# Performance work log

Measured on AMD Instinct MI355X. Metric: run time of the kernel, lower is better.

Reference implementation:

```python
import jax, jax.numpy as jnp
import numpy as np

D = 256; NH = 8; NLEV = 4; NPTS = 4; DH = D // NH
DFFN = 1024; B = 8; LQ = 900
SHAPES = np.array([[100, 100], [50, 50], [25, 25], [13, 13]], dtype=np.int64)
STARTS = np.concatenate([[0], np.cumsum(SHAPES[:, 0] * SHAPES[:, 1])[:-1]]).astype(np.int64)
LEN = int((SHAPES[:, 0] * SHAPES[:, 1]).sum())


def _ln(x, w, b, eps=1e-5):
    m = x.mean(-1, keepdims=True)
    v = ((x - m) ** 2).mean(-1, keepdims=True)
    return (x - m) / jnp.sqrt(v + eps) * w + b


def _msdeform(q, ref, src, val_w, val_b, off_w, off_b, aw_w, aw_b, op_w, op_b):
    # Multi-scale deformable attention (Deformable DETR core), grid_sample
    # bilinear / zeros padding / align_corners=False semantics.
    Bq, Lq = q.shape[0], q.shape[1]
    value = (src @ val_w + val_b).reshape(Bq, -1, NH, DH)
    off = (q @ off_w + off_b).reshape(Bq, Lq, NH, NLEV, NPTS, 2)
    aw = jax.nn.softmax((q @ aw_w + aw_b).reshape(Bq, Lq, NH, NLEV * NPTS), -1)
    aw = aw.reshape(Bq, Lq, NH, NLEV, NPTS)
    norm = jnp.asarray(SHAPES[:, ::-1].copy(), dtype=q.dtype)  # (W_l, H_l)
    loc = ref[:, :, None, :, None, :] + off / norm[None, None, None, :, None, :]
    out = jnp.zeros((Bq, Lq, NH, DH), q.dtype)
    for l in range(NLEV):
        Hl, Wl = int(SHAPES[l, 0]), int(SHAPES[l, 1]); s = int(STARTS[l])
        v = value[:, s:s + Hl * Wl]                  # [B, Hl*Wl, NH, DH]
        lx = loc[:, :, :, l, :, 0] * Wl - 0.5        # align_corners=False pixel coords
        ly = loc[:, :, :, l, :, 1] * Hl - 0.5        # [B, Lq, NH, NPTS]
        x0 = jnp.floor(lx); y0 = jnp.floor(ly)
        fx = lx - x0; fy = ly - y0
        x0 = x0.astype(jnp.int32); y0 = y0.astype(jnp.int32)
        samp = jnp.zeros((Bq, Lq, NH, NPTS, DH), q.dtype)
        for dx, dy in ((0, 0), (1, 0), (0, 1), (1, 1)):
            xi = x0 + dx; yi = y0 + dy
            w = (fx if dx else 1.0 - fx) * (fy if dy else 1.0 - fy)
            valid = (xi >= 0) & (xi < Wl) & (yi >= 0) & (yi < Hl)
            idx = jnp.clip(yi, 0, Hl - 1) * Wl + jnp.clip(xi, 0, Wl - 1)
            idx_f = idx.transpose(0, 1, 3, 2).reshape(Bq, Lq * NPTS, NH)
            g = jnp.take_along_axis(v, idx_f[..., None], axis=1)
            g = g.reshape(Bq, Lq, NPTS, NH, DH).transpose(0, 1, 3, 2, 4)
            samp = samp + jnp.where(valid, w, 0.0)[..., None] * g
        out = out + jnp.sum(samp * aw[:, :, :, l, :, None], axis=3)
    return out.reshape(Bq, Lq, D) @ op_w + op_b


def _forward(tgt, query_pos, reference_points, src, qkv_w, qkv_b, out_w, out_b,
             ln2_w, ln2_b, val_w, val_b, off_w, off_b, aw_w, aw_b, op_w, op_b,
             ln1_w, ln1_b, w1, b1, w2, b2, ln3_w, ln3_b):
    Bq, Lq, _ = tgt.shape
    # --- self attention: q=k=tgt+pos, value=tgt (eval mode, no dropout) ---
    q = tgt + query_pos
    wq, wk, wv = qkv_w[:, :D], qkv_w[:, D:2 * D], qkv_w[:, 2 * D:]
    bq, bk, bv = qkv_b[:D], qkv_b[D:2 * D], qkv_b[2 * D:]
    qh = (q @ wq + bq).reshape(Bq, Lq, NH, DH)
    kh = (q @ wk + bk).reshape(Bq, Lq, NH, DH)
    vh = (tgt @ wv + bv).reshape(Bq, Lq, NH, DH)
    scores = jnp.einsum('bqhd,bkhd->bhqk', qh, kh) / jnp.sqrt(jnp.asarray(DH, tgt.dtype))
    attn = jax.nn.softmax(scores, -1)
    sa = jnp.einsum('bhqk,bkhd->bqhd', attn, vh).reshape(Bq, Lq, D) @ out_w + out_b
    tgt = _ln(tgt + sa, ln2_w, ln2_b)
    # --- multi-scale deformable cross attention ---
    ca = _msdeform(tgt + query_pos, reference_points, src,
                   val_w, val_b, off_w, off_b, aw_w, aw_b, op_w, op_b)
    tgt = _ln(tgt + ca, ln1_w, ln1_b)
    # --- FFN ---
    ff = jax.nn.relu(tgt @ w1 + b1) @ w2 + b2
    return _ln(tgt + ff, ln3_w, ln3_b)


def setup_inputs():
    key = jax.random.key(0)
    ks = jax.random.split(key, 16)
    s = 0.02
    return {
        'tgt': jax.random.normal(ks[0], (B, LQ, D), jnp.float32),
        'query_pos': jax.random.normal(ks[1], (B, LQ, D), jnp.float32),
        'reference_points': jax.random.uniform(ks[2], (B, LQ, NLEV, 2), jnp.float32),
        'src': jax.random.normal(ks[3], (B, LEN, D), jnp.float32),
        'spatial_shapes': jnp.asarray(SHAPES),
        'level_start_index': jnp.asarray(STARTS),
        'qkv_w': jax.random.normal(ks[4], (D, 3 * D), jnp.float32) * s,
        'qkv_b': jnp.zeros((3 * D,), jnp.float32),
        'out_w': jax.random.normal(ks[5], (D, D), jnp.float32) * s,
        'out_b': jnp.zeros((D,), jnp.float32),
        'ln2_w': jnp.ones((D,), jnp.float32), 'ln2_b': jnp.zeros((D,), jnp.float32),
        'val_w': jax.random.normal(ks[6], (D, D), jnp.float32) * s,
        'val_b': jnp.zeros((D,), jnp.float32),
        'off_w': jax.random.normal(ks[7], (D, NH * NLEV * NPTS * 2), jnp.float32) * s,
        'off_b': jax.random.normal(ks[8], (NH * NLEV * NPTS * 2,), jnp.float32) * 0.5,
        'aw_w': jax.random.normal(ks[9], (D, NH * NLEV * NPTS), jnp.float32) * s,
        'aw_b': jnp.zeros((NH * NLEV * NPTS,), jnp.float32),
        'op_w': jax.random.normal(ks[10], (D, D), jnp.float32) * s,
        'op_b': jnp.zeros((D,), jnp.float32),
        'ln1_w': jnp.ones((D,), jnp.float32), 'ln1_b': jnp.zeros((D,), jnp.float32),
        'w1': jax.random.normal(ks[11], (D, DFFN), jnp.float32) * s,
        'b1': jnp.zeros((DFFN,), jnp.float32),
        'w2': jax.random.normal(ks[12], (DFFN, D), jnp.float32) * s,
        'b2': jnp.zeros((D,), jnp.float32),
        'ln3_w': jnp.ones((D,), jnp.float32), 'ln3_b': jnp.zeros((D,), jnp.float32),
    }


def reference(tgt, query_pos, reference_points, src, spatial_shapes, level_start_index,
              qkv_w, qkv_b, out_w, out_b, ln2_w, ln2_b, val_w, val_b, off_w, off_b,
              aw_w, aw_b, op_w, op_b, ln1_w, ln1_b, w1, b1, w2, b2, ln3_w, ln3_b):
    return _forward(tgt, query_pos, reference_points, src, qkv_w, qkv_b, out_w, out_b,
                    ln2_w, ln2_b, val_w, val_b, off_w, off_b, aw_w, aw_b, op_w, op_b,
                    ln1_w, ln1_b, w1, b1, w2, b2, ln3_w, ln3_b)
```

## Files before the change

kernel.cpp:

```cpp
#include <hip/hip_runtime.h>
#include <math.h>

#define Dm    256
#define NHm   8
#define DHm   32
#define NLEVm 4
#define NPTSm 4
#define DFFNm 1024
#define Bm    8
#define LQm   900
#define LENm  13294
#define MQ    (Bm * LQm)
#define MV    (Bm * LENm)
#define MQP   7296
#define MVP   106368
#define LQP   960

typedef __attribute__((ext_vector_type(8))) short short8;
typedef __attribute__((ext_vector_type(4))) float f32x4;

__device__ __forceinline__ unsigned short f2bf(float f) {
    unsigned int b = __float_as_uint(f);
    unsigned int r = (b + 0x7FFFu + ((b >> 16) & 1u)) >> 16;
    return (unsigned short)r;
}
__device__ __forceinline__ float bf2f(unsigned short u) {
    return __uint_as_float(((unsigned int)u) << 16);
}

__global__ __launch_bounds__(256) void prep0(const float* __restrict__ tgt,
                                             const float* __restrict__ qpos,
                                             unsigned short* __restrict__ tgtb,
                                             unsigned short* __restrict__ qb,
                                             int n4, int n4pad) {
    int i = blockIdx.x * blockDim.x + threadIdx.x;
    int stride = gridDim.x * blockDim.x;
    for (; i < n4pad; i += stride) {
        ushort4 ut, uq;
        if (i < n4) {
            float4 x = reinterpret_cast<const float4*>(tgt)[i];
            float4 y = reinterpret_cast<const float4*>(qpos)[i];
            ut.x = f2bf(x.x); ut.y = f2bf(x.y); ut.z = f2bf(x.z); ut.w = f2bf(x.w);
            uq.x = f2bf(x.x + y.x); uq.y = f2bf(x.y + y.y);
            uq.z = f2bf(x.z + y.z); uq.w = f2bf(x.w + y.w);
        } else {
            ut.x = ut.y = ut.z = ut.w = 0;
            uq.x = uq.y = uq.z = uq.w = 0;
        }
        reinterpret_cast<ushort4*>(tgtb)[i] = ut;
        reinterpret_cast<ushort4*>(qb)[i] = uq;
    }
}

__global__ __launch_bounds__(256) void vtpad_kernel(unsigned short* __restrict__ vt) {
    int i = blockIdx.x * 256 + threadIdx.x;
    int row = i / 60, c = 900 + (i % 60);
    vt[(size_t)row * LQP + c] = 0;
}

__device__ __forceinline__ void wt_tile(const float* __restrict__ W,
                                        unsigned short* __restrict__ BT,
                                        int N, int K, int n0, int k0, int t,
                                        float (*tile)[65]) {
    #pragma unroll
    for (int r0 = 0; r0 < 64; r0 += 16) {
        int r = r0 + (t >> 4);
        int c = (t & 15) * 4;
        float4 v = *reinterpret_cast<const float4*>(W + (size_t)(k0 + r) * N + n0 + c);
        tile[r][c + 0] = v.x; tile[r][c + 1] = v.y; tile[r][c + 2] = v.z; tile[r][c + 3] = v.w;
    }
    __syncthreads();
    #pragma unroll
    for (int s = t; s < 512; s += 256) {
        int r = s >> 3, c8 = (s & 7) * 8;
        short8 u;
        #pragma unroll
        for (int j = 0; j < 8; ++j) u[j] = (short)f2bf(tile[c8 + j][r]);
        *reinterpret_cast<short8*>(BT + (size_t)(n0 + r) * K + k0 + c8) = u;
    }
}

__global__ __launch_bounds__(256) void wt_all(
        const float* __restrict__ qkv_w, const float* __restrict__ out_w,
        const float* __restrict__ val_w, const float* __restrict__ off_w,
        const float* __restrict__ aw_w,  const float* __restrict__ op_w,
        const float* __restrict__ w1,    const float* __restrict__ w2,
        unsigned short* __restrict__ BT_qkv, unsigned short* __restrict__ BT_out,
        unsigned short* __restrict__ BT_val, unsigned short* __restrict__ BT_off,
        unsigned short* __restrict__ BT_aw,  unsigned short* __restrict__ BT_op,
        unsigned short* __restrict__ BT_w1,  unsigned short* __restrict__ BT_w2) {
    __shared__ float tile[64][65];
    int bid = blockIdx.x;
    int t = threadIdx.x;
    const float* W; unsigned short* BT; int N, K, idx;
    if      (bid < 48)  { W = qkv_w; BT = BT_qkv; N = 768;  K = 256;  idx = bid; }
    else if (bid < 64)  { W = out_w; BT = BT_out; N = 256;  K = 256;  idx = bid - 48; }
    else if (bid < 80)  { W = val_w; BT = BT_val; N = 256;  K = 256;  idx = bid - 64; }
    else if (bid < 96)  { W = off_w; BT = BT_off; N = 256;  K = 256;  idx = bid - 80; }
    else if (bid < 104) { W = aw_w;  BT = BT_aw;  N = 128;  K = 256;  idx = bid - 96; }
    else if (bid < 120) { W = op_w;  BT = BT_op;  N = 256;  K = 256;  idx = bid - 104; }
    else if (bid < 184) { W = w1;    BT = BT_w1;  N = 1024; K = 256;  idx = bid - 120; }
    else                { W = w2;    BT = BT_w2;  N = 256;  K = 1024; idx = bid - 184; }
    int nt = N / 64;
    int n0 = (idx % nt) * 64, k0 = (idx / nt) * 64;
    wt_tile(W, BT, N, K, n0, k0, t, tile);
}

template <int RELU, int OBF>
__global__ __launch_bounds__(256) void bgemm(int M, int N, int K,
        const unsigned short* __restrict__ A,
        const unsigned short* __restrict__ BT,
        const float* __restrict__ bias, const float* __restrict__ bias2,
        float* __restrict__ Cf, float* __restrict__ Cf2,
        unsigned short* __restrict__ Cb, int ldc) {
    __shared__ __align__(16) unsigned short As[2][128 * 32];
    __shared__ __align__(16) unsigned short Bs[2][128 * 32];
    int t = threadIdx.x;
    int l = t & 63;
    int w = t >> 6;
    int row0 = blockIdx.x * 128, col0 = blockIdx.y * 128;
    int wr = (w >> 1) * 64, wc = (w & 1) * 64;
    f32x4 acc[4][4];
    #pragma unroll
    for (int m = 0; m < 4; ++m)
        #pragma unroll
        for (int n = 0; n < 4; ++n) acc[m][n] = (f32x4){0.f, 0.f, 0.f, 0.f};

    int s0 = t, s1 = t + 256;
    const unsigned short* Ag = A + (size_t)row0 * K;
    const unsigned short* Bg = BT + (size_t)col0 * K;
    const unsigned short* a0p = Ag + (size_t)(s0 >> 2) * K + (s0 & 3) * 8;
    const unsigned short* a1p = Ag + (size_t)(s1 >> 2) * K + (s1 & 3) * 8;
    const unsigned short* b0p = Bg + (size_t)(s0 >> 2) * K + (s0 & 3) * 8;
    const unsigned short* b1p = Bg + (size_t)(s1 >> 2) * K + (s1 & 3) * 8;

    short8 ra0 = *(const short8*)(a0p);
    short8 ra1 = *(const short8*)(a1p);
    short8 rb0 = *(const short8*)(b0p);
    short8 rb1 = *(const short8*)(b1p);

    int cur = 0;
    for (int k0 = 0; k0 < K; k0 += 32) {
        unsigned short* Ac = As[cur];
        unsigned short* Bc = Bs[cur];
        *(short8*)(Ac + s0 * 8) = ra0;
        *(short8*)(Ac + s1 * 8) = ra1;
        *(short8*)(Bc + s0 * 8) = rb0;
        *(short8*)(Bc + s1 * 8) = rb1;
        if (k0 + 32 < K) {
            ra0 = *(const short8*)(a0p + k0 + 32);
            ra1 = *(const short8*)(a1p + k0 + 32);
            rb0 = *(const short8*)(b0p + k0 + 32);
            rb1 = *(const short8*)(b1p + k0 + 32);
        }
        __syncthreads();
        short8 af[4], bfr[4];
        #pragma unroll
        for (int m = 0; m < 4; ++m)
            af[m] = *(const short8*)(Ac + (wr + m * 16 + (l & 15)) * 32 + (l >> 4) * 8);
        #pragma unroll
        for (int n = 0; n < 4; ++n)
            bfr[n] = *(const short8*)(Bc + (wc + n * 16 + (l & 15)) * 32 + (l >> 4) * 8);
        #pragma unroll
        for (int m = 0; m < 4; ++m)
            #pragma unroll
            for (int n = 0; n < 4; ++n)
                acc[m][n] = __builtin_amdgcn_mfma_f32_16x16x32_bf16(af[m], bfr[n], acc[m][n], 0, 0, 0);
        cur ^= 1;
    }

    int cr = (l >> 4) * 4;
    int cc = l & 15;
    #pragma unroll
    for (int m = 0; m < 4; ++m) {
        #pragma unroll
        for (int n = 0; n < 4; ++n) {
            int col = col0 + wc + n * 16 + cc;
            if (OBF == 2) {
                float bv = bias[col];
                int r0 = row0 + wr + m * 16 + cr;
                if (r0 < M) {
                    int bb = r0 / 900;
                    int q = r0 - bb * 900;
                    ushort4 u;
                    u.x = f2bf(acc[m][n][0] + bv);
                    u.y = f2bf(acc[m][n][1] + bv);
                    u.z = f2bf(acc[m][n][2] + bv);
                    u.w = f2bf(acc[m][n][3] + bv);
                    *reinterpret_cast<ushort4*>(Cb + ((size_t)(bb * 256 + col)) * LQP + q) = u;
                }
            } else if (OBF == 3) {
                float bv = (col < 256) ? bias[col] : bias2[col - 256];
                #pragma unroll
                for (int j = 0; j < 4; ++j) {
                    int r = row0 + wr + m * 16 + cr + j;
                    if (r < M) {
                        float v = acc[m][n][j] + bv;
                        if (col < 256) Cf[(size_t)r * 256 + col] = v;
                        else           Cf2[(size_t)r * 128 + (col - 256)] = v;
                    }
                }
            } else {
                float bv = bias[col];
                #pragma unroll
                for (int j = 0; j < 4; ++j) {
                    int r = row0 + wr + m * 16 + cr + j;
                    if (r < M) {
                        float v = acc[m][n][j] + bv;
                        if (RELU) v = fmaxf(v, 0.f);
                        if (OBF) Cb[(size_t)r * ldc + col] = f2bf(v);
                        else     Cf[(size_t)r * ldc + col] = v;
                    }
                }
            }
        }
    }
}

__global__ __launch_bounds__(256) void bgemm_vf(int M, int N, int K,
        const float* __restrict__ A,
        const unsigned short* __restrict__ BT,
        const float* __restrict__ bias,
        unsigned short* __restrict__ Cb, int ldc) {
    __shared__ __align__(16) unsigned short As[2][128 * 32];
    __shared__ __align__(16) unsigned short Bs[2][128 * 32];
    int t = threadIdx.x;
    int l = t & 63;
    int w = t >> 6;
    int row0 = blockIdx.x * 128, col0 = blockIdx.y * 128;
    int wr = (w >> 1) * 64, wc = (w & 1) * 64;
    f32x4 acc[4][4];
    #pragma unroll
    for (int m = 0; m < 4; ++m)
        #pragma unroll
        for (int n = 0; n < 4; ++n) acc[m][n] = (f32x4){0.f, 0.f, 0.f, 0.f};

    int s0 = t, s1 = t + 256;
    int r0c = min(row0 + (s0 >> 2), M - 1);
    int r1c = min(row0 + (s1 >> 2), M - 1);
    const float* a0p = A + (size_t)r0c * K + (s0 & 3) * 8;
    const float* a1p = A + (size_t)r1c * K + (s1 & 3) * 8;
    const unsigned short* Bg = BT + (size_t)col0 * K;
    const unsigned short* b0p = Bg + (size_t)(s0 >> 2) * K + (s0 & 3) * 8;
    const unsigned short* b1p = Bg + (size_t)(s1 >> 2) * K + (s1 & 3) * 8;

    float4 fa0 = *(const float4*)(a0p);
    float4 fa1 = *(const float4*)(a0p + 4);
    float4 fb0 = *(const float4*)(a1p);
    float4 fb1 = *(const float4*)(a1p + 4);
    short8 rb0 = *(const short8*)(b0p);
    short8 rb1 = *(const short8*)(b1p);

    int cur = 0;
    for (int k0 = 0; k0 < K; k0 += 32) {
        unsigned short* Ac = As[cur];
        unsigned short* Bc = Bs[cur];
        short8 ra0, ra1;
        ra0[0] = (short)f2bf(fa0.x); ra0[1] = (short)f2bf(fa0.y);
        ra0[2] = (short)f2bf(fa0.z); ra0[3] = (short)f2bf(fa0.w);
        ra0[4] = (short)f2bf(fa1.x); ra0[5] = (short)f2bf(fa1.y);
        ra0[6] = (short)f2bf(fa1.z); ra0[7] = (short)f2bf(fa1.w);
        ra1[0] = (short)f2bf(fb0.x); ra1[1] = (short)f2bf(fb0.y);
        ra1[2] = (short)f2bf(fb0.z); ra1[3] = (short)f2bf(fb0.w);
        ra1[4] = (short)f2bf(fb1.x); ra1[5] = (short)f2bf(fb1.y);
        ra1[6] = (short)f2bf(fb1.z); ra1[7] = (short)f2bf(fb1.w);
        *(short8*)(Ac + s0 * 8) = ra0;
        *(short8*)(Ac + s1 * 8) = ra1;
        *(short8*)(Bc + s0 * 8) = rb0;
        *(short8*)(Bc + s1 * 8) = rb1;
        if (k0 + 32 < K) {
            fa0 = *(const float4*)(a0p + k0 + 32);
            fa1 = *(const float4*)(a0p + k0 + 36);
            fb0 = *(const float4*)(a1p + k0 + 32);
            fb1 = *(const float4*)(a1p + k0 + 36);
            rb0 = *(const short8*)(b0p + k0 + 32);
            rb1 = *(const short8*)(b1p + k0 + 32);
        }
        __syncthreads();
        short8 af[4], bfr[4];
        #pragma unroll
        for (int m = 0; m < 4; ++m)
            af[m] = *(const short8*)(Ac + (wr + m * 16 + (l & 15)) * 32 + (l >> 4) * 8);
        #pragma unroll
        for (int n = 0; n < 4; ++n)
            bfr[n] = *(const short8*)(Bc + (wc + n * 16 + (l & 15)) * 32 + (l >> 4) * 8);
        #pragma unroll
        for (int m = 0; m < 4; ++m)
            #pragma unroll
            for (int n = 0; n < 4; ++n)
                acc[m][n] = __builtin_amdgcn_mfma_f32_16x16x32_bf16(af[m], bfr[n], acc[m][n], 0, 0, 0);
        cur ^= 1;
    }

    int cr = (l >> 4) * 4;
    int cc = l & 15;
    #pragma unroll
    for (int m = 0; m < 4; ++m) {
        #pragma unroll
        for (int n = 0; n < 4; ++n) {
            int col = col0 + wc + n * 16 + cc;
            float bv = bias[col];
            #pragma unroll
            for (int j = 0; j < 4; ++j) {
                int r = row0 + wr + m * 16 + cr + j;
                if (r < M)
                    Cb[(size_t)r * ldc + col] = f2bf(acc[m][n][j] + bv);
            }
        }
    }
}

__global__ __launch_bounds__(256) void flash_mfma(const unsigned short* __restrict__ qk,
                                                  const unsigned short* __restrict__ vt,
                                                  unsigned short* __restrict__ out) {
    __shared__ unsigned short P_lds[4][16][72];
    int t = threadIdx.x;
    int l = t & 63, w = t >> 6;
    int lr = l & 15, lg = l >> 4;
    int qt = blockIdx.x, h = blockIdx.y, b = blockIdx.z;
    const float scale = 0.17677669529663687f;

    short8 qf = *(const short8*)(qk + (size_t)(b * LQm + qt * 64 + w * 16 + lr) * 512 + h * 32 + lg * 8);

    f32x4 accO[2];
    accO[0] = (f32x4){0.f, 0.f, 0.f, 0.f};
    accO[1] = (f32x4){0.f, 0.f, 0.f, 0.f};
    float mrow[4] = {-1e30f, -1e30f, -1e30f, -1e30f};
    float lrow[4] = {0.f, 0.f, 0.f, 0.f};
    const f32x4 zero = (f32x4){0.f, 0.f, 0.f, 0.f};
    const unsigned short* vtb = vt + ((size_t)(b * 256 + h * 32)) * LQP;

    for (int kt = 0; kt < 15; ++kt) {
        int k0 = kt * 64;
        f32x4 sfr[4];
        #pragma unroll
        for (int ks = 0; ks < 4; ++ks) {
            short8 kf = *(const short8*)(qk + (size_t)(b * LQm + k0 + ks * 16 + lr) * 512 + 256 + h * 32 + lg * 8);
            sfr[ks] = __builtin_amdgcn_mfma_f32_16x16x32_bf16(qf, kf, zero, 0, 0, 0);
        }
        float sv[4][4];
        #pragma unroll
        for (int ks = 0; ks < 4; ++ks) {
            bool valid = (k0 + ks * 16 + lr) < LQm;
            #pragma unroll
            for (int j = 0; j < 4; ++j)
                sv[ks][j] = valid ? sfr[ks][j] * scale : -1e30f;
        }
        float tm[4], newm[4], rr[4], ps[4];
        #pragma unroll
        for (int j = 0; j < 4; ++j)
            tm[j] = fmaxf(fmaxf(sv[0][j], sv[1][j]), fmaxf(sv[2][j], sv[3][j]));
        #pragma unroll
        for (int msk = 1; msk <= 8; msk <<= 1) {
            #pragma unroll
            for (int j = 0; j < 4; ++j) tm[j] = fmaxf(tm[j], __shfl_xor(tm[j], msk));
        }
        #pragma unroll
        for (int j = 0; j < 4; ++j) {
            newm[j] = fmaxf(mrow[j], tm[j]);
            rr[j] = __expf(mrow[j] - newm[j]);
            mrow[j] = newm[j];
            ps[j] = 0.f;
        }
        float pv[4][4];
        #pragma unroll
        for (int ks = 0; ks < 4; ++ks)
            #pragma unroll
            for (int j = 0; j < 4; ++j) {
                pv[ks][j] = __expf(sv[ks][j] - newm[j]);
                ps[j] += pv[ks][j];
            }
        #pragma unroll
        for (int msk = 1; msk <= 8; msk <<= 1) {
            #pragma unroll
            for (int j = 0; j < 4; ++j) ps[j] += __shfl_xor(ps[j], msk);
        }
        #pragma unroll
        for (int j = 0; j < 4; ++j) lrow[j] = lrow[j] * rr[j] + ps[j];
        #pragma unroll
        for (int n = 0; n < 2; ++n)
            #pragma unroll
            for (int j = 0; j < 4; ++j) accO[n][j] *= rr[j];
        #pragma unroll
        for (int ks = 0; ks < 4; ++ks)
            #pragma unroll
            for (int j = 0; j < 4; ++j)
                P_lds[w][lg * 4 + j][ks * 16 + lr] = f2bf(pv[ks][j]);
        #pragma unroll
        for (int kh2 = 0; kh2 < 2; ++kh2) {
            short8 pf = *(const short8*)(&P_lds[w][lr][kh2 * 32 + lg * 8]);
            #pragma unroll
            for (int n = 0; n < 2; ++n) {
                short8 vf = *(const short8*)(vtb + (size_t)(n * 16 + lr) * LQP + k0 + kh2 * 32 + lg * 8);
                accO[n] = __builtin_amdgcn_mfma_f32_16x16x32_bf16(pf, vf, accO[n], 0, 0, 0);
            }
        }
    }
    float inv[4];
    #pragma unroll
    for (int j = 0; j < 4; ++j) inv[j] = 1.0f / lrow[j];
    #pragma unroll
    for (int n = 0; n < 2; ++n)
        #pragma unroll
        for (int j = 0; j < 4; ++j) {
            int q = qt * 64 + w * 16 + lg * 4 + j;
            if (q < LQm)
                out[(size_t)(b * LQm + q) * 256 + h * 32 + n * 16 + lr] = f2bf(accO[n][j] * inv[j]);
        }
}

template <int DUAL, int QP>
__global__ __launch_bounds__(256) void add_ln_kernel(const float* __restrict__ x,
                                                     const float* __restrict__ r,
                                                     const float* __restrict__ w,
                                                     const float* __restrict__ b,
                                                     const float* __restrict__ qpos,
                                                     float* __restrict__ out,
                                                     unsigned short* __restrict__ outb,
                                                     unsigned short* __restrict__ outq) {
    int row = blockIdx.x * 4 + (threadIdx.x >> 6);
    int lane = threadIdx.x & 63;
    size_t i4 = (size_t)row * 64 + lane;
    float4 xv = reinterpret_cast<const float4*>(x)[i4];
    float4 rv = reinterpret_cast<const float4*>(r)[i4];
    float4 v = make_float4(xv.x + rv.x, xv.y + rv.y, xv.z + rv.z, xv.w + rv.w);
    float s = v.x + v.y + v.z + v.w;
    #pragma unroll
    for (int msk = 1; msk <= 32; msk <<= 1) s += __shfl_xor(s, msk);
    float mean = s * (1.0f / Dm);
    float4 dv = make_float4(v.x - mean, v.y - mean, v.z - mean, v.w - mean);
    float sq = dv.x * dv.x + dv.y * dv.y + dv.z * dv.z + dv.w * dv.w;
    #pragma unroll
    for (int msk = 1; msk <= 32; msk <<= 1) sq += __shfl_xor(sq, msk);
    float is = rsqrtf(sq * (1.0f / Dm) + 1e-5f);
    float4 wv = reinterpret_cast<const float4*>(w)[lane];
    float4 bv = reinterpret_cast<const float4*>(b)[lane];
    float4 res = make_float4(dv.x * is * wv.x + bv.x, dv.y * is * wv.y + bv.y,
                             dv.z * is * wv.z + bv.z, dv.w * is * wv.w + bv.w);
    reinterpret_cast<float4*>(out)[i4] = res;
    if (DUAL) {
        ushort4 u;
        u.x = f2bf(res.x); u.y = f2bf(res.y); u.z = f2bf(res.z); u.w = f2bf(res.w);
        reinterpret_cast<ushort4*>(outb)[i4] = u;
    }
    if (QP) {
        float4 qv = reinterpret_cast<const float4*>(qpos)[i4];
        ushort4 u;
        u.x = f2bf(res.x + qv.x); u.y = f2bf(res.y + qv.y);
        u.z = f2bf(res.z + qv.z); u.w = f2bf(res.w + qv.w);
        reinterpret_cast<ushort4*>(outq)[i4] = u;
    }
}

__global__ __launch_bounds__(256) void msdeform_kernel(const unsigned short* __restrict__ value,
                                                       const float* __restrict__ ref,
                                                       const float* __restrict__ off,
                                                       const float* __restrict__ awl,
                                                       unsigned short* __restrict__ out) {
    const int HL[4] = {100, 50, 25, 13};
    const int ST[4] = {0, 10000, 12500, 13125};
    __shared__ float lsx[4][128], lsy[4][128], wtab[4][128];
    __shared__ float2 ctab[4][512];
    int wv = threadIdx.x >> 6, lane = threadIdx.x & 63;
    int m = blockIdx.x * 4 + wv;
    int b = m / LQm;

    #pragma unroll
    for (int e = lane; e < 128; e += 64) {
        int lev = (e >> 2) & 3;
        float rx = ref[((size_t)m * NLEVm + lev) * 2 + 0];
        float ry = ref[((size_t)m * NLEVm + lev) * 2 + 1];
        float ox = off[(size_t)m * 256 + e * 2 + 0];
        float oy = off[(size_t)m * 256 + e * 2 + 1];
        float Wf = (float)HL[lev];
        lsx[wv][e] = (rx + ox / Wf) * Wf - 0.5f;
        lsy[wv][e] = (ry + oy / Wf) * Wf - 0.5f;
        wtab[wv][e] = awl[(size_t)m * 128 + e];
    }
    __syncthreads();
    if (lane < NHm) {
        int h = lane;
        float mx = -1e30f;
        #pragma unroll
        for (int i = 0; i < 16; i++) mx = fmaxf(mx, wtab[wv][h * 16 + i]);
        float s = 0.f;
        #pragma unroll
        for (int i = 0; i < 16; i++) {
            float e = __expf(wtab[wv][h * 16 + i] - mx);
            wtab[wv][h * 16 + i] = e; s += e;
        }
        float inv = 1.0f / s;
        #pragma unroll
        for (int i = 0; i < 16; i++) wtab[wv][h * 16 + i] *= inv;
    }
    __syncthreads();
    #pragma unroll
    for (int j = 0; j < 8; ++j) {
        int e2 = lane * 8 + j;
        int c = e2 & 3, e = e2 >> 2;
        int lev = (e >> 2) & 3;
        int Wl = HL[lev];
        float lx = lsx[wv][e], ly = lsy[wv][e];
        float x0f = floorf(lx), y0f = floorf(ly);
        float fx = lx - x0f, fy = ly - y0f;
        int dx = c & 1, dy = c >> 1;
        int xi = (int)x0f + dx, yi = (int)y0f + dy;
        bool valid = (xi >= 0) && (xi < Wl) && (yi >= 0) && (yi < Wl);
        float wc = valid ? ((dx ? fx : 1.0f - fx) * (dy ? fy : 1.0f - fy)) * wtab[wv][e] : 0.f;
        int xc = min(max(xi, 0), Wl - 1), yc = min(max(yi, 0), Wl - 1);
        int row = b * LENm + ST[lev] + yc * Wl + xc;
        ctab[wv][e2] = make_float2(__int_as_float(row), wc);
    }
    __syncthreads();
    int h = lane >> 3, dg = lane & 7;
    const unsigned short* basep = value + h * 32 + dg * 4;
    float a0 = 0.f, a1 = 0.f, a2 = 0.f, a3 = 0.f;
    #pragma unroll
    for (int i = 0; i < 16; ++i) {
        #pragma unroll
        for (int c = 0; c < 4; ++c) {
            float2 cc = ctab[wv][(h * 16 + i) * 4 + c];
            int row = __float_as_int(cc.x);
            float wc = cc.y;
            ushort4 v = *reinterpret_cast<const ushort4*>(basep + (size_t)row * 256);
            a0 += wc * bf2f(v.x); a1 += wc * bf2f(v.y);
            a2 += wc * bf2f(v.z); a3 += wc * bf2f(v.w);
        }
    }
    ushort4 o;
    o.x = f2bf(a0); o.y = f2bf(a1); o.z = f2bf(a2); o.w = f2bf(a3);
    *reinterpret_cast<ushort4*>(out + (size_t)m * 256 + h * 32 + dg * 4) = o;
}

extern "C" void kernel_launch(void* const* d_in, const int* in_sizes, int n_in,
                              void* d_out, int out_size, void* d_ws, size_t ws_size,
                              hipStream_t stream) {
    const float* tgt   = (const float*)d_in[0];
    const float* qpos  = (const float*)d_in[1];
    const float* refp  = (const float*)d_in[2];
    const float* src   = (const float*)d_in[3];
    const float* qkv_w = (const float*)d_in[6];
    const float* qkv_b = (const float*)d_in[7];
    const float* out_w = (const float*)d_in[8];
    const float* out_b = (const float*)d_in[9];
    const float* ln2_w = (const float*)d_in[10];
    const float* ln2_b = (const float*)d_in[11];
    const float* val_w = (const float*)d_in[12];
    const float* val_b = (const float*)d_in[13];
    const float* off_w = (const float*)d_in[14];
    const float* off_b = (const float*)d_in[15];
    const float* aw_w  = (const float*)d_in[16];
    const float* aw_b  = (const float*)d_in[17];
    const float* op_w  = (const float*)d_in[18];
    const float* op_b  = (const float*)d_in[19];
    const float* ln1_w = (const float*)d_in[20];
    const float* ln1_b = (const float*)d_in[21];
    const float* w1    = (const float*)d_in[22];
    const float* b1    = (const float*)d_in[23];
    const float* w2    = (const float*)d_in[24];
    const float* b2    = (const float*)d_in[25];
    const float* ln3_w = (const float*)d_in[26];
    const float* ln3_b = (const float*)d_in[27];

    char* base = (char*)d_ws;
    unsigned short* value_bf  = (unsigned short*)(base);
    unsigned short* hidden_bf = (unsigned short*)(base + 54460416);
    unsigned short* t2_bf     = (unsigned short*)(base + 54460416 + 14942208);
    unsigned short* qk_bf = (unsigned short*)(base + 108920832);
    float* offb = (float*)(base + 108920832);
    float* awb  = (float*)(base + 108920832 + 7372800);
    unsigned short* Vt = (unsigned short*)(base + 123666432);
    float* S1   = (float*)(base + 123666432);
    float* t1   = (float*)(base + 131039232);
    float* t2   = (float*)(base + 138412032);
    unsigned short* Qbf     = (unsigned short*)(base + 145784832);
    unsigned short* tgt_bf  = (unsigned short*)(base + 149520384);
    unsigned short* attn_bf = (unsigned short*)(base + 153255936);
    unsigned short* ca_bf   = (unsigned short*)(base + 156991488);
    unsigned short* BT_qkv  = (unsigned short*)(base + 160727040);
    unsigned short* BT_out  = BT_qkv + 768 * 256;
    unsigned short* BT_val  = BT_out + 256 * 256;
    unsigned short* BT_off  = BT_val + 256 * 256;
    unsigned short* BT_aw   = BT_off + 256 * 256;
    unsigned short* BT_op   = BT_aw + 128 * 256;
    unsigned short* BT_w1   = BT_op + 256 * 256;
    unsigned short* BT_w2   = BT_w1 + 1024 * 256;
    float* outp = (float*)d_out;

    dim3 blk(256);
    wt_all<<<dim3(248), blk, 0, stream>>>(qkv_w, out_w, val_w, off_w, aw_w, op_w, w1, w2,
                                          BT_qkv, BT_out, BT_val, BT_off, BT_aw, BT_op, BT_w1, BT_w2);

    prep0<<<dim3(1824), blk, 0, stream>>>(tgt, qpos, tgt_bf, Qbf, MQ * Dm / 4, MQP * Dm / 4);

    bgemm<0, 1><<<dim3(57, 4), blk, 0, stream>>>(MQ, 512, 256, Qbf, BT_qkv, qkv_b, nullptr, nullptr, nullptr, qk_bf, 512);
    bgemm<0, 2><<<dim3(57, 2), blk, 0, stream>>>(MQ, 256, 256, tgt_bf, BT_qkv + 512 * 256, qkv_b + 512, nullptr, nullptr, nullptr, Vt, 256);
    vtpad_kernel<<<dim3(480), blk, 0, stream>>>(Vt);
    flash_mfma<<<dim3(15, NHm, Bm), blk, 0, stream>>>(qk_bf, Vt, attn_bf);
    bgemm<0, 0><<<dim3(57, 2), blk, 0, stream>>>(MQ, 256, 256, attn_bf, BT_out, out_b, nullptr, S1, nullptr, nullptr, 256);
    add_ln_kernel<0, 1><<<dim3(1800), blk, 0, stream>>>(tgt, S1, ln2_w, ln2_b, qpos, t1, nullptr, Qbf);
    bgemm_vf<<<dim3(831, 2), blk, 0, stream>>>(MV, 256, 256, src, BT_val, val_b, value_bf, 256);
    bgemm<0, 3><<<dim3(57, 3), blk, 0, stream>>>(MQ, 384, 256, Qbf, BT_off, off_b, aw_b, offb, awb, nullptr, 0);
    msdeform_kernel<<<dim3(1800), blk, 0, stream>>>(value_bf, refp, offb, awb, ca_bf);
    bgemm<0, 0><<<dim3(57, 2), blk, 0, stream>>>(MQ, 256, 256, ca_bf, BT_op, op_b, nullptr, S1, nullptr, nullptr, 256);
    add_ln_kernel<1, 0><<<dim3(1800), blk, 0, stream>>>(t1, S1, ln1_w, ln1_b, nullptr, t2, t2_bf, nullptr);
    bgemm<1, 1><<<dim3(57, 8), blk, 0, stream>>>(MQ, DFFNm, 256, t2_bf, BT_w1, b1, nullptr, nullptr, nullptr, hidden_bf, DFFNm);
    bgemm<0, 0><<<dim3(57, 2), blk, 0, stream>>>(MQ, 256, 1024, hidden_bf, BT_w2, b2, nullptr, S1, nullptr, nullptr, 256);
    add_ln_kernel<0, 0><<<dim3(1800), blk, 0, stream>>>(t2, S1, ln3_w, ln3_b, nullptr, outp, nullptr, nullptr);
}
```

Before: 265.9 us.

## Merge value, QK, V-transpose GEMMs and Vt padding into one launch

Combines the large value projection GEMM, the Q/K projection GEMM, the transposed V projection GEMM, and the Vt padding zeroing into a single kernel that dispatches on block index. This removes three kernel launches and lets the small QK/V GEMMs share the GPU with the big value GEMM, filling otherwise underutilised CUs. The value GEMM is moved earlier in the schedule, since it does not depend on the self-attention branch. The cost is a larger, more register-heavy kernel with divergent roles per block.

```diff
diff --git a/kernel.cpp b/kernel.cpp
--- a/kernel.cpp
+++ b/kernel.cpp
@@ -50,12 +50,6 @@
         reinterpret_cast<ushort4*>(tgtb)[i] = ut;
         reinterpret_cast<ushort4*>(qb)[i] = uq;
     }
-}
-
-__global__ __launch_bounds__(256) void vtpad_kernel(unsigned short* __restrict__ vt) {
-    int i = blockIdx.x * 256 + threadIdx.x;
-    int row = i / 60, c = 900 + (i % 60);
-    vt[(size_t)row * LQP + c] = 0;
 }
 
 __device__ __forceinline__ void wt_tile(const float* __restrict__ W,
@@ -106,6 +100,22 @@
     wt_tile(W, BT, N, K, n0, k0, t, tile);
 }
 
+__device__ __forceinline__ void mfma_step(const unsigned short* Ac, const unsigned short* Bc,
+                                          int wr, int wc, int l, f32x4 acc[4][4]) {
+    short8 af[4], bfr[4];
+    #pragma unroll
+    for (int m = 0; m < 4; ++m)
+        af[m] = *(const short8*)(Ac + (wr + m * 16 + (l & 15)) * 32 + (l >> 4) * 8);
+    #pragma unroll
+    for (int n = 0; n < 4; ++n)
+        bfr[n] = *(const short8*)(Bc + (wc + n * 16 + (l & 15)) * 32 + (l >> 4) * 8);
+    #pragma unroll
+    for (int m = 0; m < 4; ++m)
+        #pragma unroll
+        for (int n = 0; n < 4; ++n)
+            acc[m][n] = __builtin_amdgcn_mfma_f32_16x16x32_bf16(af[m], bfr[n], acc[m][n], 0, 0, 0);
+}
+
 template <int RELU, int OBF>
 __global__ __launch_bounds__(256) void bgemm(int M, int N, int K,
         const unsigned short* __restrict__ A,
@@ -154,18 +164,7 @@
             rb1 = *(const short8*)(b1p + k0 + 32);
         }
         __syncthreads();
-        short8 af[4], bfr[4];
-        #pragma unroll
-        for (int m = 0; m < 4; ++m)
-            af[m] = *(const short8*)(Ac + (wr + m * 16 + (l & 15)) * 32 + (l >> 4) * 8);
-        #pragma unroll
-        for (int n = 0; n < 4; ++n)
-            bfr[n] = *(const short8*)(Bc + (wc + n * 16 + (l & 15)) * 32 + (l >> 4) * 8);
-        #pragma unroll
-        for (int m = 0; m < 4; ++m)
-            #pragma unroll
-            for (int n = 0; n < 4; ++n)
-                acc[m][n] = __builtin_amdgcn_mfma_f32_16x16x32_bf16(af[m], bfr[n], acc[m][n], 0, 0, 0);
+        mfma_step(Ac, Bc, wr, wc, l, acc);
         cur ^= 1;
     }
 
@@ -176,20 +175,7 @@
         #pragma unroll
         for (int n = 0; n < 4; ++n) {
             int col = col0 + wc + n * 16 + cc;
-            if (OBF == 2) {
-                float bv = bias[col];
-                int r0 = row0 + wr + m * 16 + cr;
-                if (r0 < M) {
-                    int bb = r0 / 900;
-                    int q = r0 - bb * 900;
-                    ushort4 u;
-                    u.x = f2bf(acc[m][n][0] + bv);
-                    u.y = f2bf(acc[m][n][1] + bv);
-                    u.z = f2bf(acc[m][n][2] + bv);
-                    u.w = f2bf(acc[m][n][3] + bv);
-                    *reinterpret_cast<ushort4*>(Cb + ((size_t)(bb * 256 + col)) * LQP + q) = u;
-                }
-            } else if (OBF == 3) {
+            if (OBF == 3) {
                 float bv = (col < 256) ? bias[col] : bias2[col - 256];
                 #pragma unroll
                 for (int j = 0; j < 4; ++j) {
@@ -217,94 +203,169 @@
     }
 }
 
-__global__ __launch_bounds__(256) void bgemm_vf(int M, int N, int K,
-        const float* __restrict__ A,
-        const unsigned short* __restrict__ BT,
-        const float* __restrict__ bias,
-        unsigned short* __restrict__ Cb, int ldc) {
+__global__ __launch_bounds__(256) void fused_gemms(
+        const float* __restrict__ src, const unsigned short* __restrict__ BT_val,
+        const float* __restrict__ val_b, unsigned short* __restrict__ value_bf,
+        const unsigned short* __restrict__ Qbf, const unsigned short* __restrict__ BT_qkv,
+        const float* __restrict__ qkv_b, unsigned short* __restrict__ qk_bf,
+        const unsigned short* __restrict__ tgt_bf, unsigned short* __restrict__ Vt) {
     __shared__ __align__(16) unsigned short As[2][128 * 32];
     __shared__ __align__(16) unsigned short Bs[2][128 * 32];
+    int bid = blockIdx.x;
     int t = threadIdx.x;
-    int l = t & 63;
-    int w = t >> 6;
-    int row0 = blockIdx.x * 128, col0 = blockIdx.y * 128;
+
+    if (bid >= 2004) {
+        int i = (bid - 2004) * 256 + t;
+        int row = i / 60, c = 900 + (i % 60);
+        Vt[(size_t)row * LQP + c] = 0;
+        return;
+    }
+
+    int l = t & 63, w = t >> 6;
     int wr = (w >> 1) * 64, wc = (w & 1) * 64;
+    int s0 = t, s1 = t + 256;
     f32x4 acc[4][4];
     #pragma unroll
     for (int m = 0; m < 4; ++m)
         #pragma unroll
         for (int n = 0; n < 4; ++n) acc[m][n] = (f32x4){0.f, 0.f, 0.f, 0.f};
-
-    int s0 = t, s1 = t + 256;
-    int r0c = min(row0 + (s0 >> 2), M - 1);
-    int r1c = min(row0 + (s1 >> 2), M - 1);
-    const float* a0p = A + (size_t)r0c * K + (s0 & 3) * 8;
-    const float* a1p = A + (size_t)r1c * K + (s1 & 3) * 8;
-    const unsigned short* Bg = BT + (size_t)col0 * K;
-    const unsigned short* b0p = Bg + (size_t)(s0 >> 2) * K + (s0 & 3) * 8;
-    const unsigned short* b1p = Bg + (size_t)(s1 >> 2) * K + (s1 & 3) * 8;
-
-    float4 fa0 = *(const float4*)(a0p);
-    float4 fa1 = *(const float4*)(a0p + 4);
-    float4 fb0 = *(const float4*)(a1p);
-    float4 fb1 = *(const float4*)(a1p + 4);
-    short8 rb0 = *(const short8*)(b0p);
-    short8 rb1 = *(const short8*)(b1p);
-
-    int cur = 0;
-    for (int k0 = 0; k0 < K; k0 += 32) {
-        unsigned short* Ac = As[cur];
-        unsigned short* Bc = Bs[cur];
-        short8 ra0, ra1;
-        ra0[0] = (short)f2bf(fa0.x); ra0[1] = (short)f2bf(fa0.y);
-        ra0[2] = (short)f2bf(fa0.z); ra0[3] = (short)f2bf(fa0.w);
-        ra0[4] = (short)f2bf(fa1.x); ra0[5] = (short)f2bf(fa1.y);
-        ra0[6] = (short)f2bf(fa1.z); ra0[7] = (short)f2bf(fa1.w);
-        ra1[0] = (short)f2bf(fb0.x); ra1[1] = (short)f2bf(fb0.y);
-        ra1[2] = (short)f2bf(fb0.z); ra1[3] = (short)f2bf(fb0.w);
-        ra1[4] = (short)f2bf(fb1.x); ra1[5] = (short)f2bf(fb1.y);
-        ra1[6] = (short)f2bf(fb1.z); ra1[7] = (short)f2bf(fb1.w);
-        *(short8*)(Ac + s0 * 8) = ra0;
-        *(short8*)(Ac + s1 * 8) = ra1;
-        *(short8*)(Bc + s0 * 8) = rb0;
-        *(short8*)(Bc + s1 * 8) = rb1;
-        if (k0 + 32 < K) {
-            fa0 = *(const float4*)(a0p + k0 + 32);
-            fa1 = *(const float4*)(a0p + k0 + 36);
-            fb0 = *(const float4*)(a1p + k0 + 32);
-            fb1 = *(const float4*)(a1p + k0 + 36);
-            rb0 = *(const short8*)(b0p + k0 + 32);
-            rb1 = *(const short8*)(b1p + k0 + 32);
-        }
-        __syncthreads();
-        short8 af[4], bfr[4];
-        #pragma unroll
-        for (int m = 0; m < 4; ++m)
-            af[m] = *(const short8*)(Ac + (wr + m * 16 + (l & 15)) * 32 + (l >> 4) * 8);
-        #pragma unroll
-        for (int n = 0; n < 4; ++n)
-            bfr[n] = *(const short8*)(Bc + (wc + n * 16 + (l & 15)) * 32 + (l >> 4) * 8);
-        #pragma unroll
-        for (int m = 0; m < 4; ++m)
-            #pragma unroll
-            for (int n = 0; n < 4; ++n)
-                acc[m][n] = __builtin_amdgcn_mfma_f32_16x16x32_bf16(af[m], bfr[n], acc[m][n], 0, 0, 0);
-        cur ^= 1;
-    }
-
     int cr = (l >> 4) * 4;
     int cc = l & 15;
-    #pragma unroll
-    for (int m = 0; m < 4; ++m) {
-        #pragma unroll
-        for (int n = 0; n < 4; ++n) {
-            int col = col0 + wc + n * 16 + cc;
-            float bv = bias[col];
-            #pragma unroll
-            for (int j = 0; j < 4; ++j) {
-                int r = row0 + wr + m * 16 + cr + j;
-                if (r < M)
-                    Cb[(size_t)r * ldc + col] = f2bf(acc[m][n][j] + bv);
+
+    if (bid < 1662) {
+        int row0 = (bid % 831) * 128, col0 = (bid / 831) * 128;
+        int r0c = min(row0 + (s0 >> 2), MV - 1);
+        int r1c = min(row0 + (s1 >> 2), MV - 1);
+        const float* a0p = src + (size_t)r0c * 256 + (s0 & 3) * 8;
+        const float* a1p = src + (size_t)r1c * 256 + (s1 & 3) * 8;
+        const unsigned short* Bg = BT_val + (size_t)col0 * 256;
+        const unsigned short* b0p = Bg + (size_t)(s0 >> 2) * 256 + (s0 & 3) * 8;
+        const unsigned short* b1p = Bg + (size_t)(s1 >> 2) * 256 + (s1 & 3) * 8;
+
+        float4 fa0 = *(const float4*)(a0p);
+        float4 fa1 = *(const float4*)(a0p + 4);
+        float4 fb0 = *(const float4*)(a1p);
+        float4 fb1 = *(const float4*)(a1p + 4);
+        short8 rb0 = *(const short8*)(b0p);
+        short8 rb1 = *(const short8*)(b1p);
+
+        int cur = 0;
+        for (int k0 = 0; k0 < 256; k0 += 32) {
+            unsigned short* Ac = As[cur];
+            unsigned short* Bc = Bs[cur];
+            short8 ra0, ra1;
+            ra0[0] = (short)f2bf(fa0.x); ra0[1] = (short)f2bf(fa0.y);
+            ra0[2] = (short)f2bf(fa0.z); ra0[3] = (short)f2bf(fa0.w);
+            ra0[4] = (short)f2bf(fa1.x); ra0[5] = (short)f2bf(fa1.y);
+            ra0[6] = (short)f2bf(fa1.z); ra0[7] = (short)f2bf(fa1.w);
+            ra1[0] = (short)f2bf(fb0.x); ra1[1] = (short)f2bf(fb0.y);
+            ra1[2] = (short)f2bf(fb0.z); ra1[3] = (short)f2bf(fb0.w);
+            ra1[4] = (short)f2bf(fb1.x); ra1[5] = (short)f2bf(fb1.y);
+            ra1[6] = (short)f2bf(fb1.z); ra1[7] = (short)f2bf(fb1.w);
+            *(short8*)(Ac + s0 * 8) = ra0;
+            *(short8*)(Ac + s1 * 8) = ra1;
+            *(short8*)(Bc + s0 * 8) = rb0;
+            *(short8*)(Bc + s1 * 8) = rb1;
+            if (k0 + 32 < 256) {
+                fa0 = *(const float4*)(a0p + k0 + 32);
+                fa1 = *(const float4*)(a0p + k0 + 36);
+                fb0 = *(const float4*)(a1p + k0 + 32);
+                fb1 = *(const float4*)(a1p + k0 + 36);
+                rb0 = *(const short8*)(b0p + k0 + 32);
+                rb1 = *(const short8*)(b1p + k0 + 32);
+            }
+            __syncthreads();
+            mfma_step(Ac, Bc, wr, wc, l, acc);
+            cur ^= 1;
+        }
+        #pragma unroll
+        for (int m = 0; m < 4; ++m) {
+            #pragma unroll
+            for (int n = 0; n < 4; ++n) {
+                int col = col0 + wc + n * 16 + cc;
+                float bv = val_b[col];
+                #pragma unroll
+                for (int j = 0; j < 4; ++j) {
+                    int r = row0 + wr + m * 16 + cr + j;
+                    if (r < MV)
+                        value_bf[(size_t)r * 256 + col] = f2bf(acc[m][n][j] + bv);
+                }
+            }
+        }
+    } else {
+        bool is_qk = (bid < 1890);
+        int idx = is_qk ? (bid - 1662) : (bid - 1890);
+        int row0 = (idx % 57) * 128;
+        int col0 = (idx / 57) * 128;
+        const unsigned short* A  = is_qk ? Qbf : tgt_bf;
+        const unsigned short* BT = is_qk ? BT_qkv : (BT_qkv + 512 * 256);
+        const float* bias        = is_qk ? qkv_b : (qkv_b + 512);
+
+        const unsigned short* Ag = A + (size_t)row0 * 256;
+        const unsigned short* Bg = BT + (size_t)col0 * 256;
+        const unsigned short* a0p = Ag + (size_t)(s0 >> 2) * 256 + (s0 & 3) * 8;
+        const unsigned short* a1p = Ag + (size_t)(s1 >> 2) * 256 + (s1 & 3) * 8;
+        const unsigned short* b0p = Bg + (size_t)(s0 >> 2) * 256 + (s0 & 3) * 8;
+        const unsigned short* b1p = Bg + (size_t)(s1 >> 2) * 256 + (s1 & 3) * 8;
+
+        short8 ra0 = *(const short8*)(a0p);
+        short8 ra1 = *(const short8*)(a1p);
+        short8 rb0 = *(const short8*)(b0p);
+        short8 rb1 = *(const short8*)(b1p);
+
+        int cur = 0;
+        for (int k0 = 0; k0 < 256; k0 += 32) {
+            unsigned short* Ac = As[cur];
+            unsigned short* Bc = Bs[cur];
+            *(short8*)(Ac + s0 * 8) = ra0;
+            *(short8*)(Ac + s1 * 8) = ra1;
+            *(short8*)(Bc + s0 * 8) = rb0;
+            *(short8*)(Bc + s1 * 8) = rb1;
+            if (k0 + 32 < 256) {
+                ra0 = *(const short8*)(a0p + k0 + 32);
+                ra1 = *(const short8*)(a1p + k0 + 32);
+                rb0 = *(const short8*)(b0p + k0 + 32);
+                rb1 = *(const short8*)(b1p + k0 + 32);
+            }
+            __syncthreads();
+            mfma_step(Ac, Bc, wr, wc, l, acc);
+            cur ^= 1;
+        }
+
+        if (is_qk) {
+            #pragma unroll
+            for (int m = 0; m < 4; ++m) {
+                #pragma unroll
+                for (int n = 0; n < 4; ++n) {
+                    int col = col0 + wc + n * 16 + cc;
+                    float bv = bias[col];
+                    #pragma unroll
+                    for (int j = 0; j < 4; ++j) {
+                        int r = row0 + wr + m * 16 + cr + j;
+                        if (r < MQ)
+                            qk_bf[(size_t)r * 512 + col] = f2bf(acc[m][n][j] + bv);
+                    }
+                }
+            }
+        } else {
+            #pragma unroll
+            for (int m = 0; m < 4; ++m) {
+                #pragma unroll
+                for (int n = 0; n < 4; ++n) {
+                    int col = col0 + wc + n * 16 + cc;
+                    float bv = bias[col];
+                    int r0 = row0 + wr + m * 16 + cr;
+                    if (r0 < MQ) {
+                        int bb = r0 / 900;
+                        int q = r0 - bb * 900;
+                        ushort4 u;
+                        u.x = f2bf(acc[m][n][0] + bv);
+                        u.y = f2bf(acc[m][n][1] + bv);
+                        u.z = f2bf(acc[m][n][2] + bv);
+                        u.w = f2bf(acc[m][n][3] + bv);
+                        *reinterpret_cast<ushort4*>(Vt + ((size_t)(bb * 256 + col)) * LQP + q) = u;
+                    }
+                }
             }
         }
     }
@@ -590,16 +651,14 @@
     dim3 blk(256);
     wt_all<<<dim3(248), blk, 0, stream>>>(qkv_w, out_w, val_w, off_w, aw_w, op_w, w1, w2,
                                           BT_qkv, BT_out, BT_val, BT_off, BT_aw, BT_op, BT_w1, BT_w2);
-
     prep0<<<dim3(1824), blk, 0, stream>>>(tgt, qpos, tgt_bf, Qbf, MQ * Dm / 4, MQP * Dm / 4);
 
-    bgemm<0, 1><<<dim3(57, 4), blk, 0, stream>>>(MQ, 512, 256, Qbf, BT_qkv, qkv_b, nullptr, nullptr, nullptr, qk_bf, 512);
-    bgemm<0, 2><<<dim3(57, 2), blk, 0, stream>>>(MQ, 256, 256, tgt_bf, BT_qkv + 512 * 256, qkv_b + 512, nullptr, nullptr, nullptr, Vt, 256);
-    vtpad_kernel<<<dim3(480), blk, 0, stream>>>(Vt);
+    fused_gemms<<<dim3(2484), blk, 0, stream>>>(src, BT_val, val_b, value_bf,
+                                                Qbf, BT_qkv, qkv_b, qk_bf, tgt_bf, Vt);
+
     flash_mfma<<<dim3(15, NHm, Bm), blk, 0, stream>>>(qk_bf, Vt, attn_bf);
     bgemm<0, 0><<<dim3(57, 2), blk, 0, stream>>>(MQ, 256, 256, attn_bf, BT_out, out_b, nullptr, S1, nullptr, nullptr, 256);
     add_ln_kernel<0, 1><<<dim3(1800), blk, 0, stream>>>(tgt, S1, ln2_w, ln2_b, qpos, t1, nullptr, Qbf);
-    bgemm_vf<<<dim3(831, 2), blk, 0, stream>>>(MV, 256, 256, src, BT_val, val_b, value_bf, 256);
     bgemm<0, 3><<<dim3(57, 3), blk, 0, stream>>>(MQ, 384, 256, Qbf, BT_off, off_b, aw_b, offb, awb, nullptr, 0);
     msdeform_kernel<<<dim3(1800), blk, 0, stream>>>(value_bf, refp, offb, awb, ca_bf);
     bgemm<0, 0><<<dim3(57, 2), blk, 0, stream>>>(MQ, 256, 256, ca_bf, BT_op, op_b, nullptr, S1, nullptr, nullptr, 256);
```

Result: faster. 251.4 us (-5.4%).
